# Kernel tuning notes

Measured on AMD Instinct MI355X. Metric: run time of the kernel, lower is better.

Reference implementation:

```python
import jax, jax.numpy as jnp
import numpy as np

KERNEL_SIZE = 3

def setup_inputs() -> dict:
    key = jax.random.key(0)
    k1, k2, k3, k4, k5 = jax.random.split(key, 5)
    B, L, D, K = 4, 4096, 1024, KERNEL_SIZE
    x = jax.random.normal(k1, (B, L, D), dtype=jnp.float32)
    # depthwise conv: torch weight shape (D, 1, K) -> store as (D, K)
    fan_dw = 1.0 / np.sqrt(1 * K)
    w_dw = jax.random.uniform(k2, (D, K), dtype=jnp.float32, minval=-fan_dw, maxval=fan_dw)
    b_dw = jax.random.uniform(k3, (D,), dtype=jnp.float32, minval=-fan_dw, maxval=fan_dw)
    # pointwise conv: torch weight shape (D, D, 1) -> store as (D_out, D_in)
    fan_pw = 1.0 / np.sqrt(D * 1)
    w_pw = jax.random.uniform(k4, (D, D), dtype=jnp.float32, minval=-fan_pw, maxval=fan_pw)
    b_pw = jax.random.uniform(k5, (D,), dtype=jnp.float32, minval=-fan_pw, maxval=fan_pw)
    return {"x": x, "w_dw": w_dw, "b_dw": b_dw, "w_pw": w_pw, "b_pw": b_pw}

def _causal_dw_pw(x, w_dw, b_dw, w_pw, b_pw):
    # x: (B, L, D); causal left-pad by K-1 along L
    K = w_dw.shape[1]
    L = x.shape[1]
    xp = jnp.pad(x, ((0, 0), (K - 1, 0), (0, 0)))  # (B, L+K-1, D)
    # depthwise: y[b,l,d] = sum_k xp[b,l+k,d] * w_dw[d,k]
    y = sum(xp[:, k:k + L, :] * w_dw[:, k] for k in range(K)) + b_dw
    # pointwise 1x1 conv: mix channels
    return jnp.einsum('bld,ed->ble', y, w_pw) + b_pw

def reference(x, w_dw, b_dw, w_pw, b_pw):
    return _causal_dw_pw(x, w_dw, b_dw, w_pw, b_pw)
```

## Files before the change

kernel.cpp:

```cpp
#include <hip/hip_runtime.h>
#include <hip/hip_bf16.h>
#include <stdint.h>

#define B_SZ   4
#define L_SEQ  4096
#define D_DIM  1024
#define M_TOT  (B_SZ * L_SEQ)

typedef __bf16 bf16;
typedef __attribute__((ext_vector_type(8))) __bf16 bf16x8;
typedef __attribute__((ext_vector_type(4))) float   f32x4;

#define GLOAD_LDS16(g, l)                                                     \
  __builtin_amdgcn_global_load_lds(                                           \
      (const __attribute__((address_space(1))) void*)(g),                     \
      (__attribute__((address_space(3))) void*)(l), 16, 0, 0)

__global__ __launch_bounds__(256) void dw_bf16_kernel(
    const float* __restrict__ x, const float* __restrict__ w_dw,
    const float* __restrict__ b_dw, bf16* __restrict__ y,
    const float* __restrict__ w_pw, bf16* __restrict__ wpwb) {
  const int t = threadIdx.x;
  if (blockIdx.x >= B_SZ * (L_SEQ / 16)) {
    int i = ((blockIdx.x - B_SZ * (L_SEQ / 16)) * 256 + t) * 8;
    float4 a = *(const float4*)(w_pw + i);
    float4 b = *(const float4*)(w_pw + i + 4);
    union { bf16 h[8]; int4 v; } r;
    r.h[0] = (bf16)a.x; r.h[1] = (bf16)a.y; r.h[2] = (bf16)a.z; r.h[3] = (bf16)a.w;
    r.h[4] = (bf16)b.x; r.h[5] = (bf16)b.y; r.h[6] = (bf16)b.z; r.h[7] = (bf16)b.w;
    *(int4*)(wpwb + i) = r.v;
    return;
  }
  const int b  = blockIdx.x >> 8;
  const int l0 = (blockIdx.x & 255) * 16;
  const int d0 = t * 4;
  const float* xb = x + (size_t)b * L_SEQ * D_DIM + d0;
  bf16*        yb = y + (size_t)b * L_SEQ * D_DIM + d0;

  float4 xr[18];
  const float4 zero = make_float4(0.f, 0.f, 0.f, 0.f);
  xr[0] = (l0 >= 2) ? *(const float4*)(xb + (size_t)(l0 - 2) * D_DIM) : zero;
  xr[1] = (l0 >= 1) ? *(const float4*)(xb + (size_t)(l0 - 1) * D_DIM) : zero;
#pragma unroll
  for (int j = 0; j < 16; ++j)
    xr[j + 2] = *(const float4*)(xb + (size_t)(l0 + j) * D_DIM);

  const float* wp = w_dw + d0 * 3;
  float4 wa = *(const float4*)(wp);
  float4 wb = *(const float4*)(wp + 4);
  float4 wc = *(const float4*)(wp + 8);
  float4 bv = *(const float4*)(b_dw + d0);

#pragma unroll
  for (int j = 0; j < 16; ++j) {
    float4 x2 = xr[j], x1 = xr[j + 1], x0 = xr[j + 2];
    float a0 = fmaf(x2.x, wa.x, fmaf(x1.x, wa.y, fmaf(x0.x, wa.z, bv.x)));
    float a1 = fmaf(x2.y, wa.w, fmaf(x1.y, wb.x, fmaf(x0.y, wb.y, bv.y)));
    float a2 = fmaf(x2.z, wb.z, fmaf(x1.z, wb.w, fmaf(x0.z, wc.x, bv.z)));
    float a3 = fmaf(x2.w, wc.y, fmaf(x1.w, wc.z, fmaf(x0.w, wc.w, bv.w)));
    union { bf16 h[4]; int2 v; } o;
    o.h[0] = (bf16)a0; o.h[1] = (bf16)a1; o.h[2] = (bf16)a2; o.h[3] = (bf16)a3;
    *(int2*)(yb + (size_t)(l0 + j) * D_DIM) = o.v;
  }
}

#define BM 128
#define BN 128
#define BK 32
#define EP_ROWP 68

__global__ __launch_bounds__(256) void gemm_bt_kernel(
    const bf16* __restrict__ A,
    const bf16* __restrict__ Bm,
    const float* __restrict__ bias, float* __restrict__ C) {
  __shared__ __align__(16) char smem[32768];

  const int t    = threadIdx.x;
  const int m0   = blockIdx.x * BM;
  const int n0   = blockIdx.y * BN;
  const int lane = t & 63;
  const int wv   = t >> 6;
  const int wm   = (wv >> 1) * 64;
  const int wn   = (wv & 1) * 64;
  const int lrow = lane & 15;
  const int q    = lane >> 4;

  f32x4 acc[4][4] = {};

  int srow[2], sgc[2];
#pragma unroll
  for (int i = 0; i < 2; ++i) {
    int s   = i * 256 + t;
    srow[i] = s >> 2;
    sgc[i]  = (s & 3) ^ ((srow[i] >> 1) & 3);
  }
  const unsigned lbase = (unsigned)(wv * 1024);

  auto stage = [&](int p, int k0) {
#pragma unroll
    for (int i = 0; i < 2; ++i) {
      unsigned off = (unsigned)(p * 16384 + i * 4096) + lbase;
      GLOAD_LDS16(A  + (size_t)(m0 + srow[i]) * D_DIM + k0 + sgc[i] * 8, smem + off);
      GLOAD_LDS16(Bm + (size_t)(n0 + srow[i]) * D_DIM + k0 + sgc[i] * 8, smem + 8192 + off);
    }
  };

  stage(0, 0);
  for (int it = 0; it < D_DIM / BK; ++it) {
    __syncthreads();
    if (it < D_DIM / BK - 1) stage((it + 1) & 1, (it + 1) * BK);
    const char* Ab = smem + (it & 1) * 16384;
    const char* Bb = Ab + 8192;

    bf16x8 af[4], bfr[4];
#pragma unroll
    for (int i = 0; i < 4; ++i) {
      int mrow = wm + i * 16 + lrow;
      int ck   = q ^ ((mrow >> 1) & 3);
      af[i] = *(const bf16x8*)(Ab + (size_t)mrow * (BK * 2) + ck * 16);
      int nrow = wn + i * 16 + lrow;
      int ckb  = q ^ ((nrow >> 1) & 3);
      bfr[i] = *(const bf16x8*)(Bb + (size_t)nrow * (BK * 2) + ckb * 16);
    }
#pragma unroll
    for (int i = 0; i < 4; ++i)
#pragma unroll
      for (int j = 0; j < 4; ++j)
        acc[i][j] = __builtin_amdgcn_mfma_f32_16x16x32_bf16(af[i], bfr[j], acc[i][j], 0, 0, 0);
  }

  __syncthreads();
  float* ep = (float*)smem + (size_t)wv * (16 * EP_ROWP);

  float bvj[4];
#pragma unroll
  for (int j = 0; j < 4; ++j) bvj[j] = bias[n0 + wn + j * 16 + lrow];

#pragma unroll
  for (int i = 0; i < 4; ++i) {
#pragma unroll
    for (int j = 0; j < 4; ++j)
#pragma unroll
      for (int r = 0; r < 4; ++r)
        ep[(q * 4 + r) * EP_ROWP + j * 16 + lrow] = acc[i][j][r] + bvj[j];
#pragma unroll
    for (int it = 0; it < 4; ++it) {
      int flat = it * 64 + lane;
      int row  = flat >> 4;
      int c4   = flat & 15;
      float4 v = *(const float4*)(ep + row * EP_ROWP + c4 * 4);
      int gm = m0 + wm + i * 16 + row;
      int gn = n0 + wn + c4 * 4;
      *(float4*)(C + (size_t)gm * D_DIM + gn) = v;
    }
  }
}

__global__ __launch_bounds__(256) void fallback_kernel(
    const float* __restrict__ x, const float* __restrict__ w_dw,
    const float* __restrict__ b_dw, const float* __restrict__ w_pw,
    const float* __restrict__ b_pw, float* __restrict__ out) {
  __shared__ float ys[D_DIM];
  const int m = blockIdx.x;
  const int l = m & (L_SEQ - 1);
  const int t = threadIdx.x;
  const float* xr = x + (size_t)m * D_DIM;
#pragma unroll
  for (int c = 0; c < 4; ++c) {
    int d = t + c * 256;
    float a = fmaf(xr[d], w_dw[d * 3 + 2], b_dw[d]);
    if (l >= 1) a = fmaf(xr[d - D_DIM], w_dw[d * 3 + 1], a);
    if (l >= 2) a = fmaf(xr[d - 2 * D_DIM], w_dw[d * 3 + 0], a);
    ys[d] = a;
  }
  __syncthreads();
#pragma unroll
  for (int c = 0; c < 4; ++c) {
    int e = t + c * 256;
    const float* wr = w_pw + (size_t)e * D_DIM;
    float a = b_pw[e];
    for (int d = 0; d < D_DIM; ++d) a = fmaf(ys[d], wr[d], a);
    out[(size_t)m * D_DIM + e] = a;
  }
}

extern "C" void kernel_launch(void* const* d_in, const int* in_sizes, int n_in,
                              void* d_out, int out_size, void* d_ws, size_t ws_size,
                              hipStream_t stream) {
  (void)in_sizes; (void)n_in; (void)out_size;
  const float* x    = (const float*)d_in[0];
  const float* w_dw = (const float*)d_in[1];
  const float* b_dw = (const float*)d_in[2];
  const float* w_pw = (const float*)d_in[3];
  const float* b_pw = (const float*)d_in[4];
  float* out = (float*)d_out;

  const size_t y_elems = (size_t)M_TOT * D_DIM;
  const size_t w_elems = (size_t)D_DIM * D_DIM;
  const size_t need = (y_elems + w_elems) * sizeof(bf16);

  if (ws_size >= need) {
    bf16* y    = (bf16*)d_ws;
    bf16* wpwb = (bf16*)d_ws + y_elems;
    const int dw_blocks  = B_SZ * (L_SEQ / 16);
    const int cvt_blocks = (D_DIM * D_DIM / 8) / 256;
    dw_bf16_kernel<<<dw_blocks + cvt_blocks, 256, 0, stream>>>(x, w_dw, b_dw, y, w_pw, wpwb);
    dim3 grid(M_TOT / BM, D_DIM / BN);
    gemm_bt_kernel<<<grid, 256, 0, stream>>>(y, wpwb, b_pw, out);
  } else {
    fallback_kernel<<<M_TOT, 256, 0, stream>>>(x, w_dw, b_dw, w_pw, b_pw, out);
  }
}
```

Measured before the change: 172.2 us.

## Fuse depthwise conv and weight conversion into GEMM A/B tile staging

Removes the separate depthwise and weight-cast kernel and the bf16 workspace intermediate. Each GEMM block now loads fp32 x rows (with a two-row causal halo) and fp32 pointwise weights into registers, computes the depthwise conv, converts to bf16 and writes swizzled LDS tiles. Global loads for the next k-tile are issued before the MFMAs of the current tile. This saves the intermediate write and read, but recomputes the depthwise conv once per N-block (8x), reads fp32 data at twice the bytes, and converts the weights in every block instead of using direct global-to-LDS loads.

```diff
diff --git a/kernel.cpp b/kernel.cpp
--- a/kernel.cpp
+++ b/kernel.cpp
@@ -11,68 +11,15 @@
 typedef __attribute__((ext_vector_type(8))) __bf16 bf16x8;
 typedef __attribute__((ext_vector_type(4))) float   f32x4;
 
-#define GLOAD_LDS16(g, l)                                                     \
-  __builtin_amdgcn_global_load_lds(                                           \
-      (const __attribute__((address_space(1))) void*)(g),                     \
-      (__attribute__((address_space(3))) void*)(l), 16, 0, 0)
-
-__global__ __launch_bounds__(256) void dw_bf16_kernel(
-    const float* __restrict__ x, const float* __restrict__ w_dw,
-    const float* __restrict__ b_dw, bf16* __restrict__ y,
-    const float* __restrict__ w_pw, bf16* __restrict__ wpwb) {
-  const int t = threadIdx.x;
-  if (blockIdx.x >= B_SZ * (L_SEQ / 16)) {
-    int i = ((blockIdx.x - B_SZ * (L_SEQ / 16)) * 256 + t) * 8;
-    float4 a = *(const float4*)(w_pw + i);
-    float4 b = *(const float4*)(w_pw + i + 4);
-    union { bf16 h[8]; int4 v; } r;
-    r.h[0] = (bf16)a.x; r.h[1] = (bf16)a.y; r.h[2] = (bf16)a.z; r.h[3] = (bf16)a.w;
-    r.h[4] = (bf16)b.x; r.h[5] = (bf16)b.y; r.h[6] = (bf16)b.z; r.h[7] = (bf16)b.w;
-    *(int4*)(wpwb + i) = r.v;
-    return;
-  }
-  const int b  = blockIdx.x >> 8;
-  const int l0 = (blockIdx.x & 255) * 16;
-  const int d0 = t * 4;
-  const float* xb = x + (size_t)b * L_SEQ * D_DIM + d0;
-  bf16*        yb = y + (size_t)b * L_SEQ * D_DIM + d0;
-
-  float4 xr[18];
-  const float4 zero = make_float4(0.f, 0.f, 0.f, 0.f);
-  xr[0] = (l0 >= 2) ? *(const float4*)(xb + (size_t)(l0 - 2) * D_DIM) : zero;
-  xr[1] = (l0 >= 1) ? *(const float4*)(xb + (size_t)(l0 - 1) * D_DIM) : zero;
-#pragma unroll
-  for (int j = 0; j < 16; ++j)
-    xr[j + 2] = *(const float4*)(xb + (size_t)(l0 + j) * D_DIM);
-
-  const float* wp = w_dw + d0 * 3;
-  float4 wa = *(const float4*)(wp);
-  float4 wb = *(const float4*)(wp + 4);
-  float4 wc = *(const float4*)(wp + 8);
-  float4 bv = *(const float4*)(b_dw + d0);
-
-#pragma unroll
-  for (int j = 0; j < 16; ++j) {
-    float4 x2 = xr[j], x1 = xr[j + 1], x0 = xr[j + 2];
-    float a0 = fmaf(x2.x, wa.x, fmaf(x1.x, wa.y, fmaf(x0.x, wa.z, bv.x)));
-    float a1 = fmaf(x2.y, wa.w, fmaf(x1.y, wb.x, fmaf(x0.y, wb.y, bv.y)));
-    float a2 = fmaf(x2.z, wb.z, fmaf(x1.z, wb.w, fmaf(x0.z, wc.x, bv.z)));
-    float a3 = fmaf(x2.w, wc.y, fmaf(x1.w, wc.z, fmaf(x0.w, wc.w, bv.w)));
-    union { bf16 h[4]; int2 v; } o;
-    o.h[0] = (bf16)a0; o.h[1] = (bf16)a1; o.h[2] = (bf16)a2; o.h[3] = (bf16)a3;
-    *(int2*)(yb + (size_t)(l0 + j) * D_DIM) = o.v;
-  }
-}
-
 #define BM 128
 #define BN 128
 #define BK 32
 #define EP_ROWP 68
 
-__global__ __launch_bounds__(256) void gemm_bt_kernel(
-    const bf16* __restrict__ A,
-    const bf16* __restrict__ Bm,
-    const float* __restrict__ bias, float* __restrict__ C) {
+__global__ __launch_bounds__(256) void fused_dwpw_gemm(
+    const float* __restrict__ x, const float* __restrict__ w_dw,
+    const float* __restrict__ b_dw, const float* __restrict__ w_pw,
+    const float* __restrict__ b_pw, float* __restrict__ C) {
   __shared__ __align__(16) char smem[32768];
 
   const int t    = threadIdx.x;
@@ -85,56 +32,114 @@
   const int lrow = lane & 15;
   const int q    = lane >> 4;
 
+  const int cg = t & 7;
+  const int rg = t >> 3;
+  const int c4 = cg * 4;
+  const int r0 = rg * 4;
+
+  unsigned wr[4];
+#pragma unroll
+  for (int j = 0; j < 4; ++j) {
+    int row = r0 + j;
+    unsigned a = (unsigned)(row * 64) +
+                 ((((unsigned)(cg >> 1)) ^ ((unsigned)((row >> 1) & 3))) << 4) +
+                 ((unsigned)(cg & 1) << 3);
+    a ^= ((unsigned)((row >> 2) & 1)) << 6;
+    wr[j] = a;
+  }
+  unsigned ra[4], rb[4];
+#pragma unroll
+  for (int i = 0; i < 4; ++i) {
+    int mrow = wm + i * 16 + lrow;
+    unsigned a = (unsigned)(mrow * 64) +
+                 (((unsigned)q ^ (unsigned)((mrow >> 1) & 3)) << 4);
+    a ^= ((unsigned)((mrow >> 2) & 1)) << 6;
+    ra[i] = a;
+    int nrow = wn + i * 16 + lrow;
+    unsigned b2 = (unsigned)(nrow * 64) +
+                  (((unsigned)q ^ (unsigned)((nrow >> 1) & 3)) << 4);
+    b2 ^= ((unsigned)((nrow >> 2) & 1)) << 6;
+    rb[i] = b2;
+  }
+
+  const bool edge = (r0 == 0) && ((m0 & (L_SEQ - 1)) == 0);
+  const float* xbase = x + (size_t)(m0 + r0 - 2) * D_DIM + c4;
+  const float* bbase = w_pw + (size_t)(n0 + r0) * D_DIM + c4;
+
   f32x4 acc[4][4] = {};
 
-  int srow[2], sgc[2];
+  float4 xa[6], bw4[4], wwa, wwb, wwc, bv;
+
+  auto issue = [&](int k0) {
+    const float4 zero = make_float4(0.f, 0.f, 0.f, 0.f);
+    const float* xp = xbase + k0;
+    xa[0] = edge ? zero : *(const float4*)(xp);
+    xa[1] = edge ? zero : *(const float4*)(xp + D_DIM);
 #pragma unroll
-  for (int i = 0; i < 2; ++i) {
-    int s   = i * 256 + t;
-    srow[i] = s >> 2;
-    sgc[i]  = (s & 3) ^ ((srow[i] >> 1) & 3);
-  }
-  const unsigned lbase = (unsigned)(wv * 1024);
+    for (int j = 2; j < 6; ++j) xa[j] = *(const float4*)(xp + (size_t)j * D_DIM);
+    const float* bp = bbase + k0;
+#pragma unroll
+    for (int j = 0; j < 4; ++j) bw4[j] = *(const float4*)(bp + (size_t)j * D_DIM);
+    const float* wp = w_dw + (size_t)(k0 + c4) * 3;
+    wwa = *(const float4*)(wp);
+    wwb = *(const float4*)(wp + 4);
+    wwc = *(const float4*)(wp + 8);
+    bv  = *(const float4*)(b_dw + k0 + c4);
+  };
 
-  auto stage = [&](int p, int k0) {
+  auto convert_store = [&](int p) {
+    char* Ab = smem + p * 16384;
+    char* Bb = Ab + 8192;
 #pragma unroll
-    for (int i = 0; i < 2; ++i) {
-      unsigned off = (unsigned)(p * 16384 + i * 4096) + lbase;
-      GLOAD_LDS16(A  + (size_t)(m0 + srow[i]) * D_DIM + k0 + sgc[i] * 8, smem + off);
-      GLOAD_LDS16(Bm + (size_t)(n0 + srow[i]) * D_DIM + k0 + sgc[i] * 8, smem + 8192 + off);
+    for (int j = 0; j < 4; ++j) {
+      float4 x2 = xa[j], x1 = xa[j + 1], x0 = xa[j + 2];
+      float a0 = fmaf(x2.x, wwa.x, fmaf(x1.x, wwa.y, fmaf(x0.x, wwa.z, bv.x)));
+      float a1 = fmaf(x2.y, wwa.w, fmaf(x1.y, wwb.x, fmaf(x0.y, wwb.y, bv.y)));
+      float a2 = fmaf(x2.z, wwb.z, fmaf(x1.z, wwb.w, fmaf(x0.z, wwc.x, bv.z)));
+      float a3 = fmaf(x2.w, wwc.y, fmaf(x1.w, wwc.z, fmaf(x0.w, wwc.w, bv.w)));
+      union { bf16 h[4]; int2 v; } o;
+      o.h[0] = (bf16)a0; o.h[1] = (bf16)a1; o.h[2] = (bf16)a2; o.h[3] = (bf16)a3;
+      *(int2*)(Ab + wr[j]) = o.v;
+    }
+#pragma unroll
+    for (int j = 0; j < 4; ++j) {
+      union { bf16 h[4]; int2 v; } o;
+      o.h[0] = (bf16)bw4[j].x; o.h[1] = (bf16)bw4[j].y;
+      o.h[2] = (bf16)bw4[j].z; o.h[3] = (bf16)bw4[j].w;
+      *(int2*)(Bb + wr[j]) = o.v;
     }
   };
 
-  stage(0, 0);
+  issue(0);
+  convert_store(0);
+  __syncthreads();
+
   for (int it = 0; it < D_DIM / BK; ++it) {
-    __syncthreads();
-    if (it < D_DIM / BK - 1) stage((it + 1) & 1, (it + 1) * BK);
+    if (it + 1 < D_DIM / BK) issue((it + 1) * BK);
+
     const char* Ab = smem + (it & 1) * 16384;
     const char* Bb = Ab + 8192;
-
     bf16x8 af[4], bfr[4];
 #pragma unroll
     for (int i = 0; i < 4; ++i) {
-      int mrow = wm + i * 16 + lrow;
-      int ck   = q ^ ((mrow >> 1) & 3);
-      af[i] = *(const bf16x8*)(Ab + (size_t)mrow * (BK * 2) + ck * 16);
-      int nrow = wn + i * 16 + lrow;
-      int ckb  = q ^ ((nrow >> 1) & 3);
-      bfr[i] = *(const bf16x8*)(Bb + (size_t)nrow * (BK * 2) + ckb * 16);
+      af[i]  = *(const bf16x8*)(Ab + ra[i]);
+      bfr[i] = *(const bf16x8*)(Bb + rb[i]);
     }
 #pragma unroll
     for (int i = 0; i < 4; ++i)
 #pragma unroll
       for (int j = 0; j < 4; ++j)
         acc[i][j] = __builtin_amdgcn_mfma_f32_16x16x32_bf16(af[i], bfr[j], acc[i][j], 0, 0, 0);
+
+    if (it + 1 < D_DIM / BK) convert_store((it + 1) & 1);
+    __syncthreads();
   }
 
-  __syncthreads();
   float* ep = (float*)smem + (size_t)wv * (16 * EP_ROWP);
 
   float bvj[4];
 #pragma unroll
-  for (int j = 0; j < 4; ++j) bvj[j] = bias[n0 + wn + j * 16 + lrow];
+  for (int j = 0; j < 4; ++j) bvj[j] = b_pw[n0 + wn + j * 16 + lrow];
 
 #pragma unroll
   for (int i = 0; i < 4; ++i) {
@@ -144,50 +149,22 @@
       for (int r = 0; r < 4; ++r)
         ep[(q * 4 + r) * EP_ROWP + j * 16 + lrow] = acc[i][j][r] + bvj[j];
 #pragma unroll
-    for (int it = 0; it < 4; ++it) {
-      int flat = it * 64 + lane;
+    for (int it2 = 0; it2 < 4; ++it2) {
+      int flat = it2 * 64 + lane;
       int row  = flat >> 4;
-      int c4   = flat & 15;
-      float4 v = *(const float4*)(ep + row * EP_ROWP + c4 * 4);
+      int c16  = flat & 15;
+      float4 v = *(const float4*)(ep + row * EP_ROWP + c16 * 4);
       int gm = m0 + wm + i * 16 + row;
-      int gn = n0 + wn + c4 * 4;
+      int gn = n0 + wn + c16 * 4;
       *(float4*)(C + (size_t)gm * D_DIM + gn) = v;
     }
-  }
-}
-
-__global__ __launch_bounds__(256) void fallback_kernel(
-    const float* __restrict__ x, const float* __restrict__ w_dw,
-    const float* __restrict__ b_dw, const float* __restrict__ w_pw,
-    const float* __restrict__ b_pw, float* __restrict__ out) {
-  __shared__ float ys[D_DIM];
-  const int m = blockIdx.x;
-  const int l = m & (L_SEQ - 1);
-  const int t = threadIdx.x;
-  const float* xr = x + (size_t)m * D_DIM;
-#pragma unroll
-  for (int c = 0; c < 4; ++c) {
-    int d = t + c * 256;
-    float a = fmaf(xr[d], w_dw[d * 3 + 2], b_dw[d]);
-    if (l >= 1) a = fmaf(xr[d - D_DIM], w_dw[d * 3 + 1], a);
-    if (l >= 2) a = fmaf(xr[d - 2 * D_DIM], w_dw[d * 3 + 0], a);
-    ys[d] = a;
-  }
-  __syncthreads();
-#pragma unroll
-  for (int c = 0; c < 4; ++c) {
-    int e = t + c * 256;
-    const float* wr = w_pw + (size_t)e * D_DIM;
-    float a = b_pw[e];
-    for (int d = 0; d < D_DIM; ++d) a = fmaf(ys[d], wr[d], a);
-    out[(size_t)m * D_DIM + e] = a;
   }
 }
 
 extern "C" void kernel_launch(void* const* d_in, const int* in_sizes, int n_in,
                               void* d_out, int out_size, void* d_ws, size_t ws_size,
                               hipStream_t stream) {
-  (void)in_sizes; (void)n_in; (void)out_size;
+  (void)in_sizes; (void)n_in; (void)out_size; (void)d_ws; (void)ws_size;
   const float* x    = (const float*)d_in[0];
   const float* w_dw = (const float*)d_in[1];
   const float* b_dw = (const float*)d_in[2];
@@ -195,19 +172,6 @@
   const float* b_pw = (const float*)d_in[4];
   float* out = (float*)d_out;
 
-  const size_t y_elems = (size_t)M_TOT * D_DIM;
-  const size_t w_elems = (size_t)D_DIM * D_DIM;
-  const size_t need = (y_elems + w_elems) * sizeof(bf16);
-
-  if (ws_size >= need) {
-    bf16* y    = (bf16*)d_ws;
-    bf16* wpwb = (bf16*)d_ws + y_elems;
-    const int dw_blocks  = B_SZ * (L_SEQ / 16);
-    const int cvt_blocks = (D_DIM * D_DIM / 8) / 256;
-    dw_bf16_kernel<<<dw_blocks + cvt_blocks, 256, 0, stream>>>(x, w_dw, b_dw, y, w_pw, wpwb);
-    dim3 grid(M_TOT / BM, D_DIM / BN);
-    gemm_bt_kernel<<<grid, 256, 0, stream>>>(y, wpwb, b_pw, out);
-  } else {
-    fallback_kernel<<<M_TOT, 256, 0, stream>>>(x, w_dw, b_dw, w_pw, b_pw, out);
-  }
+  dim3 grid(M_TOT / BM, D_DIM / BN);
+  fused_dwpw_gemm<<<grid, 256, 0, stream>>>(x, w_dw, b_dw, w_pw, b_pw, out);
 }
```

Measured after the change: 233.2 us. 35.4% more time.

## Replace 128x128 GEMM with 256x256 tile, 4-stage async LDS pipeline

Applied to the files above, without the earlier changes.

Replaces the double-buffered 128x128 bf16 GEMM with a 512-thread kernel computing 256x256 tiles. It uses a 4-deep ring of direct global-to-LDS loads paced by explicit vmcnt waits, and interleaves the A and B prefetches between two MFMA halves. It also adds an extra XOR swizzle bit for LDS bank spreading and raises wave priority during MFMA bursts. The goals are more operand reuse per LDS byte and hiding global latency. The costs are 128KB of shared memory per block, a grid of only 256 blocks, and heavier register pressure.

```diff
diff --git a/kernel.cpp b/kernel.cpp
--- a/kernel.cpp
+++ b/kernel.cpp
@@ -64,93 +64,135 @@
   }
 }
 
-#define BM 128
-#define BN 128
-#define BK 32
 #define EP_ROWP 68
 
-__global__ __launch_bounds__(256) void gemm_bt_kernel(
+__global__ __launch_bounds__(512, 2) void gemm256_kernel(
     const bf16* __restrict__ A,
     const bf16* __restrict__ Bm,
     const float* __restrict__ bias, float* __restrict__ C) {
-  __shared__ __align__(16) char smem[32768];
+  __shared__ __align__(16) char smem[131072];
 
   const int t    = threadIdx.x;
-  const int m0   = blockIdx.x * BM;
-  const int n0   = blockIdx.y * BN;
+  const int m0   = blockIdx.x * 256;
+  const int n0   = blockIdx.y * 256;
   const int lane = t & 63;
   const int wv   = t >> 6;
-  const int wm   = (wv >> 1) * 64;
-  const int wn   = (wv & 1) * 64;
+  const int wmh  = wv >> 2;
+  const int wn   = wv & 3;
   const int lrow = lane & 15;
   const int q    = lane >> 4;
 
-  f32x4 acc[4][4] = {};
-
-  int srow[2], sgc[2];
-#pragma unroll
-  for (int i = 0; i < 2; ++i) {
-    int s   = i * 256 + t;
-    srow[i] = s >> 2;
-    sgc[i]  = (s & 3) ^ ((srow[i] >> 1) & 3);
+  unsigned ra[8], rb[4];
+#pragma unroll
+  for (int i = 0; i < 8; ++i) {
+    int row = wmh * 128 + i * 16 + lrow;
+    unsigned a = (unsigned)(row * 64) +
+                 ((((unsigned)q) ^ ((unsigned)((row >> 1) & 3))) << 4);
+    a ^= ((unsigned)((row >> 2) & 1)) << 6;
+    ra[i] = a;
+  }
+#pragma unroll
+  for (int j = 0; j < 4; ++j) {
+    int row = wn * 64 + j * 16 + lrow;
+    unsigned a = (unsigned)(row * 64) +
+                 ((((unsigned)q) ^ ((unsigned)((row >> 1) & 3))) << 4);
+    a ^= ((unsigned)((row >> 2) & 1)) << 6;
+    rb[j] = a;
+  }
+
+  const bf16* agp[2];
+  const bf16* bgp[2];
+#pragma unroll
+  for (int r = 0; r < 2; ++r) {
+    int rs = r * 128 + (t >> 2);
+    int grow = rs ^ ((rs >> 2) & 1);
+    int gc   = (t & 3) ^ ((rs >> 1) & 3);
+    agp[r] = A  + (size_t)(m0 + grow) * D_DIM + gc * 8;
+    bgp[r] = Bm + (size_t)(n0 + grow) * D_DIM + gc * 8;
   }
   const unsigned lbase = (unsigned)(wv * 1024);
 
-  auto stage = [&](int p, int k0) {
-#pragma unroll
-    for (int i = 0; i < 2; ++i) {
-      unsigned off = (unsigned)(p * 16384 + i * 4096) + lbase;
-      GLOAD_LDS16(A  + (size_t)(m0 + srow[i]) * D_DIM + k0 + sgc[i] * 8, smem + off);
-      GLOAD_LDS16(Bm + (size_t)(n0 + srow[i]) * D_DIM + k0 + sgc[i] * 8, smem + 8192 + off);
-    }
+  auto stageA = [&](int kt) {
+    unsigned bb = (unsigned)((kt & 3) * 32768);
+#pragma unroll
+    for (int r = 0; r < 2; ++r)
+      GLOAD_LDS16(agp[r] + kt * 32, smem + bb + r * 8192 + lbase);
   };
-
-  stage(0, 0);
-  for (int it = 0; it < D_DIM / BK; ++it) {
-    __syncthreads();
-    if (it < D_DIM / BK - 1) stage((it + 1) & 1, (it + 1) * BK);
-    const char* Ab = smem + (it & 1) * 16384;
-    const char* Bb = Ab + 8192;
-
-    bf16x8 af[4], bfr[4];
-#pragma unroll
-    for (int i = 0; i < 4; ++i) {
-      int mrow = wm + i * 16 + lrow;
-      int ck   = q ^ ((mrow >> 1) & 3);
-      af[i] = *(const bf16x8*)(Ab + (size_t)mrow * (BK * 2) + ck * 16);
-      int nrow = wn + i * 16 + lrow;
-      int ckb  = q ^ ((nrow >> 1) & 3);
-      bfr[i] = *(const bf16x8*)(Bb + (size_t)nrow * (BK * 2) + ckb * 16);
-    }
+  auto stageB = [&](int kt) {
+    unsigned bb = (unsigned)((kt & 3) * 32768 + 16384);
+#pragma unroll
+    for (int r = 0; r < 2; ++r)
+      GLOAD_LDS16(bgp[r] + kt * 32, smem + bb + r * 8192 + lbase);
+  };
+
+  f32x4 acc[8][4] = {};
+
+  stageA(0); stageB(0);
+  stageA(1); stageB(1);
+  stageA(2); stageB(2);
+
+  for (int kt = 0; kt < 32; ++kt) {
+    if (kt < 30)       asm volatile("s_waitcnt vmcnt(8)" ::: "memory");
+    else if (kt == 30) asm volatile("s_waitcnt vmcnt(4)" ::: "memory");
+    else               asm volatile("s_waitcnt vmcnt(0)" ::: "memory");
+    __builtin_amdgcn_s_barrier();
+
+    const char* Ab = smem + (size_t)((kt & 3) * 32768);
+    const char* Bb = Ab + 16384;
+
+    bf16x8 af[4], bfr[4], af2[4];
+#pragma unroll
+    for (int i = 0; i < 4; ++i) af[i]  = *(const bf16x8*)(Ab + ra[i]);
+#pragma unroll
+    for (int j = 0; j < 4; ++j) bfr[j] = *(const bf16x8*)(Bb + rb[j]);
+    if (kt <= 28) stageA(kt + 3);
+    __builtin_amdgcn_sched_barrier(0);
+    __builtin_amdgcn_s_barrier();
+    __builtin_amdgcn_s_setprio(1);
 #pragma unroll
     for (int i = 0; i < 4; ++i)
 #pragma unroll
       for (int j = 0; j < 4; ++j)
         acc[i][j] = __builtin_amdgcn_mfma_f32_16x16x32_bf16(af[i], bfr[j], acc[i][j], 0, 0, 0);
-  }
-
-  __syncthreads();
+    __builtin_amdgcn_s_setprio(0);
+    __builtin_amdgcn_sched_barrier(0);
+    __builtin_amdgcn_s_barrier();
+
+#pragma unroll
+    for (int i = 0; i < 4; ++i) af2[i] = *(const bf16x8*)(Ab + ra[4 + i]);
+    if (kt <= 28) stageB(kt + 3);
+    __builtin_amdgcn_sched_barrier(0);
+    __builtin_amdgcn_s_barrier();
+    __builtin_amdgcn_s_setprio(1);
+#pragma unroll
+    for (int i = 0; i < 4; ++i)
+#pragma unroll
+      for (int j = 0; j < 4; ++j)
+        acc[4 + i][j] = __builtin_amdgcn_mfma_f32_16x16x32_bf16(af2[i], bfr[j], acc[4 + i][j], 0, 0, 0);
+    __builtin_amdgcn_s_setprio(0);
+  }
+
   float* ep = (float*)smem + (size_t)wv * (16 * EP_ROWP);
 
   float bvj[4];
 #pragma unroll
-  for (int j = 0; j < 4; ++j) bvj[j] = bias[n0 + wn + j * 16 + lrow];
-
-#pragma unroll
-  for (int i = 0; i < 4; ++i) {
+  for (int j = 0; j < 4; ++j) bvj[j] = bias[n0 + wn * 64 + j * 16 + lrow];
+
+#pragma unroll
+  for (int i = 0; i < 8; ++i) {
 #pragma unroll
     for (int j = 0; j < 4; ++j)
 #pragma unroll
       for (int r = 0; r < 4; ++r)
         ep[(q * 4 + r) * EP_ROWP + j * 16 + lrow] = acc[i][j][r] + bvj[j];
 #pragma unroll
-    for (int it = 0; it < 4; ++it) {
-      int flat = it * 64 + lane;
+    for (int it2 = 0; it2 < 4; ++it2) {
+      int flat = it2 * 64 + lane;
       int row  = flat >> 4;
-      int c4   = flat & 15;
-      float4 v = *(const float4*)(ep + row * EP_ROWP + c4 * 4);
-      int gm = m0 + wm + i * 16 + row;
-      int gn = n0 + wn + c4 * 4;
+      int c16  = flat & 15;
+      float4 v = *(const float4*)(ep + row * EP_ROWP + c16 * 4);
+      int gm = m0 + wmh * 128 + i * 16 + row;
+      int gn = n0 + wn * 64 + c16 * 4;
       *(float4*)(C + (size_t)gm * D_DIM + gn) = v;
     }
   }
@@ -205,8 +247,8 @@
     const int dw_blocks  = B_SZ * (L_SEQ / 16);
     const int cvt_blocks = (D_DIM * D_DIM / 8) / 256;
     dw_bf16_kernel<<<dw_blocks + cvt_blocks, 256, 0, stream>>>(x, w_dw, b_dw, y, w_pw, wpwb);
-    dim3 grid(M_TOT / BM, D_DIM / BN);
-    gemm_bt_kernel<<<grid, 256, 0, stream>>>(y, wpwb, b_pw, out);
+    dim3 grid(M_TOT / 256, D_DIM / 256);
+    gemm256_kernel<<<grid, 512, 0, stream>>>(y, wpwb, b_pw, out);
   } else {
     fallback_kernel<<<M_TOT, 256, 0, stream>>>(x, w_dw, b_dw, w_pw, b_pw, out);
   }
```

After: 155.4 us. 1.11x faster.
